# Optimization experiments

Hardware: AMD Instinct MI355X
Metric: run time of the kernel (lower is better)

## Reference

```python
import jax, jax.numpy as jnp
import numpy as np

N_QUBITS = 16
NUM_CLASSES = 16
C64 = jnp.complex64


def rx_mat(theta):
    # RX(theta) = [[cos(t/2), -i sin(t/2)], [-i sin(t/2), cos(t/2)]]
    c = jnp.cos(theta / 2).astype(C64)
    s = jnp.sin(theta / 2).astype(C64)
    row0 = jnp.stack([c, -1j * s], axis=-1)
    row1 = jnp.stack([-1j * s, c], axis=-1)
    return jnp.stack([row0, row1], axis=-2)  # (..., 2, 2)


def rot_mat(phi, theta, omega):
    # PennyLane Rot = RZ(omega) RY(theta) RZ(phi)
    c = jnp.cos(theta / 2).astype(C64)
    s = jnp.sin(theta / 2).astype(C64)
    phi = phi.astype(C64)
    omega = omega.astype(C64)
    e_m = jnp.exp(-0.5j * (phi + omega))
    e_p = jnp.exp(0.5j * (phi + omega))
    e_d = jnp.exp(0.5j * (phi - omega))
    e_dm = jnp.exp(-0.5j * (phi - omega))
    return jnp.array([[e_m * c, -e_d * s], [e_dm * s, e_p * c]], dtype=C64)


def apply_1q(state, U, w):
    # state: (B, 2, ..., 2) with qubit w at axis 1+w; U: (2,2) or (B,2,2)
    s = jnp.moveaxis(state, 1 + w, -1)
    if U.ndim == 3:
        s = jnp.einsum('b...i,bji->b...j', s, U)
    else:
        s = jnp.einsum('...i,ji->...j', s, U)
    return jnp.moveaxis(s, -1, 1 + w)


def apply_crx(state, theta, ctrl, tgt):
    U = rx_mat(theta)  # (2, 2)
    s = jnp.moveaxis(state, (1 + ctrl, 1 + tgt), (-2, -1))
    s1 = jnp.einsum('...i,ji->...j', s[..., 1, :], U)
    s = jnp.stack([s[..., 0, :], s1], axis=-2)
    return jnp.moveaxis(s, (-2, -1), (1 + ctrl, 1 + tgt))


def circuit(feats, rot1, crx1, rot2, crx2):
    # feats: (B, 16) rotation angles (data re-uploading)
    B = feats.shape[0]
    state = jnp.zeros((B,) + (2,) * N_QUBITS, dtype=C64)
    state = state.at[(slice(None),) + (0,) * N_QUBITS].set(1.0)

    def layer(state, rot_w, crx_w):
        for i in range(N_QUBITS):
            state = apply_1q(state, rx_mat(feats[:, i]), i)  # batched RX
        for i in range(N_QUBITS):
            state = apply_1q(state, rot_mat(rot_w[i, 0], rot_w[i, 1], rot_w[i, 2]), i)
        for i in range(N_QUBITS):
            state = apply_crx(state, crx_w[i], i, (i + 1) % N_QUBITS)
        return state

    state = layer(state, rot1, crx1)
    state = layer(state, rot2, crx2)

    probs = (state.real ** 2 + state.imag ** 2)  # (B, 2, ..., 2) float32
    evs = []
    for i in range(N_QUBITS):
        p = jnp.moveaxis(probs, 1 + i, 1).reshape(B, 2, -1).sum(-1)
        evs.append(p[:, 0] - p[:, 1])  # <Z_i>
    return jnp.stack(evs, axis=1)  # (B, 16)


def adaptive_pool_441(x):
    # AdaptiveAvgPool3d((4,4,1)) with divisible dims -> block means
    B, C, D, H, W = x.shape
    x = x.reshape(B, C, 4, D // 4, 4, H // 4, 1, W)
    return x.mean(axis=(3, 5, 7))  # (B, C, 4, 4, 1)


def setup_inputs() -> dict:
    key = jax.random.key(0)
    ks = jax.random.split(key, 9)
    B = 128
    x = jax.random.normal(ks[0], (B, 2, 16, 64, 64), dtype=jnp.float32)
    compress_w = jax.random.normal(ks[1], (N_QUBITS, 32), jnp.float32) * 0.1
    compress_b = jax.random.normal(ks[2], (N_QUBITS,), jnp.float32) * 0.01
    rot1 = jax.random.normal(ks[3], (N_QUBITS, 3), jnp.float32) * 0.1
    crx1 = jax.random.normal(ks[4], (N_QUBITS,), jnp.float32) * 0.1
    rot2 = jax.random.normal(ks[5], (N_QUBITS, 3), jnp.float32) * 0.1
    crx2 = jax.random.normal(ks[6], (N_QUBITS,), jnp.float32) * 0.1
    fc_w = jax.random.normal(ks[7], (NUM_CLASSES, N_QUBITS), jnp.float32) * 0.1
    fc_b = jax.random.normal(ks[8], (NUM_CLASSES,), jnp.float32) * 0.01
    return {"x": x, "compress_w": compress_w, "compress_b": compress_b,
            "rot1": rot1, "crx1": crx1, "rot2": rot2, "crx2": crx2,
            "fc_w": fc_w, "fc_b": fc_b}


def reference(x, compress_w, compress_b, rot1, crx1, rot2, crx2, fc_w, fc_b):
    B = x.shape[0]
    p = adaptive_pool_441(x).reshape(B, -1)          # (B, 32)
    feats = p @ compress_w.T + compress_b            # (B, 16)
    q_out = circuit(feats, rot1, crx1, rot2, crx2)   # (B, 16)
    logits = q_out @ fc_w.T + fc_b                   # (B, 16)
    return jax.nn.log_softmax(logits, axis=1)
```

## Files before the change

kernel.cpp:

```cpp
#include <hip/hip_runtime.h>
#include <hip/hip_bf16.h>

typedef float f2 __attribute__((ext_vector_type(2)));

__device__ __forceinline__ f2 sgate(f2 a, int lane, int kt, int kc, const float* u) {
    f2 p;
    p.x = __shfl_xor(a.x, 1 << kt);
    p.y = __shfl_xor(a.y, 1 << kt);
    const float* uu = u + ((kc >= 0 && ((lane >> kc) & 1)) ? 8 : 0);
    int bit = (lane >> kt) & 1;
    float cAr = bit ? uu[6] : uu[0], cAi = bit ? uu[7] : uu[1];
    float cPr = bit ? uu[4] : uu[2], cPi = bit ? uu[5] : uu[3];
    f2 r;
    r.x = cAr * a.x - cAi * a.y + cPr * p.x - cPi * p.y;
    r.y = cAr * a.y + cAi * a.x + cPr * p.y + cPi * p.x;
    return r;
}

__device__ __forceinline__ f2 cmul(f2 A, f2 B) {
    return f2{A.x * B.x - A.y * B.y, A.x * B.y + A.y * B.x};
}
__device__ __forceinline__ f2 cmulc(f2 x, f2 y) {
    return f2{x.x * y.x + x.y * y.y, x.y * y.x - x.x * y.y};
}

__global__ __launch_bounds__(256) void pool_kernel(const float* __restrict__ x,
                                                   float* __restrict__ p) {
    int blk = blockIdx.x;
    int b = blk >> 5, j = blk & 31;
    int c = j >> 4, dd = (j >> 2) & 3, hh = j & 3;
    const float4* xb = (const float4*)(x + (((size_t)(b * 2 + c) * 16 + dd * 4) << 12)
                                         + (size_t)hh * 1024);
    int tid = threadIdx.x;
    float sum = 0.f;
    #pragma unroll
    for (int k = 0; k < 4; ++k) {
        int f = k * 256 + tid;
        int r = f >> 4, col = f & 15;
        int off = (r >> 4) * 1024 + (r & 15) * 16 + col;
        float4 v = xb[off];
        sum += v.x + v.y + v.z + v.w;
    }
    #pragma unroll
    for (int o = 1; o < 64; o <<= 1) sum += __shfl_xor(sum, o);
    __shared__ float red[4];
    if ((tid & 63) == 0) red[tid >> 6] = sum;
    __syncthreads();
    if (tid == 0) p[blk] = (red[0] + red[1] + red[2] + red[3]) * (1.0f / 4096.0f);
}

__global__ __launch_bounds__(256) void qfin(const float* __restrict__ p,
                                            const float* __restrict__ cw,
                                            const float* __restrict__ cb,
                                            const float* __restrict__ rot1,
                                            const float* __restrict__ crx1,
                                            const float* __restrict__ rot2,
                                            const float* __restrict__ crx2,
                                            const float* __restrict__ fcw,
                                            const float* __restrict__ fcb,
                                            float* __restrict__ out) {
    __shared__ float pp[32];
    __shared__ float uM[32][16];
    __shared__ float cs15[4];
    __shared__ f2 ell[64];
    __shared__ f2 Rr[2][64];
    __shared__ f2 Wl[2][32];
    __shared__ f2 Btab[4][64];
    __shared__ f2 Ctab[8][32];
    __shared__ float Rtab[2][4][64];
    __shared__ float sH[2][6][32];
    __shared__ float sD[2][32];
    __shared__ float sE[2][32];
    __shared__ float redP[4][7];
    __shared__ float redQ[4][8];
    __shared__ float evf[16];
    __shared__ float lgf[16];
    int tid = threadIdx.x;
    int b = blockIdx.x;

    if (tid < 32) pp[tid] = p[b * 32 + tid];
    __syncthreads();

    if (tid < 32) {
        int q = tid & 15, l = tid >> 4;
        float f = cb[q];
        #pragma unroll
        for (int jj = 0; jj < 32; ++jj) f += pp[jj] * cw[q * 32 + jj];
        float cr = cosf(0.5f * f), sr = sinf(0.5f * f);
        const float* rw = (l == 0 ? rot1 : rot2) + q * 3;
        float phi = rw[0], th = rw[1], om = rw[2];
        float ct = cosf(0.5f * th), st = sinf(0.5f * th);
        float aa = 0.5f * (phi + om), dd = 0.5f * (phi - om);
        float ca = cosf(aa), sa = sinf(aa), cd = cosf(dd), sd = sinf(dd);
        float R00r =  ct * ca, R00i = -ct * sa;
        float R01r = -st * cd, R01i = -st * sd;
        float R10r =  st * cd, R10i = -st * sd;
        float R11r =  ct * ca, R11i =  ct * sa;
        float u0 = cr * R00r + sr * R01i;
        float u1 = cr * R00i - sr * R01r;
        float u2 = cr * R01r + sr * R00i;
        float u3 = cr * R01i - sr * R00r;
        float u4 = cr * R10r + sr * R11i;
        float u5 = cr * R10i - sr * R11r;
        float u6 = cr * R11r + sr * R10i;
        float u7 = cr * R11i - sr * R10r;
        float g[16];
        g[0] = u0; g[1] = u1; g[2] = u2; g[3] = u3;
        g[4] = u4; g[5] = u5; g[6] = u6; g[7] = u7;
        if (q >= 1) {
            float thc = (l == 0 ? crx1 : crx2)[q - 1];
            float c2 = cosf(0.5f * thc), s2 = sinf(0.5f * thc);
            g[8]  = c2*u0 + s2*u5;  g[9]  = c2*u1 - s2*u4;
            g[10] = c2*u2 + s2*u7;  g[11] = c2*u3 - s2*u6;
            g[12] = c2*u4 + s2*u1;  g[13] = c2*u5 - s2*u0;
            g[14] = c2*u6 + s2*u3;  g[15] = c2*u7 - s2*u2;
        } else {
            #pragma unroll
            for (int k = 0; k < 8; ++k) g[8 + k] = g[k];
        }
        float* s = uM[l * 16 + q];
        #pragma unroll
        for (int k = 0; k < 16; ++k) s[k] = g[k];
        if (q == 15) {
            float th2 = (l == 0 ? crx1 : crx2)[15];
            cs15[l * 2]     = cosf(0.5f * th2);
            cs15[l * 2 + 1] = sinf(0.5f * th2);
        }
    }
    __syncthreads();

    int wv = tid >> 6, lane = tid & 63;

    if (wv == 0) {
        f2 a = (lane == 0) ? f2{1.f, 0.f} : f2{0.f, 0.f};
        a = sgate(a, lane, 0, -1, uM[0]);
        #pragma unroll
        for (int q = 1; q <= 5; ++q) a = sgate(a, lane, q, q - 1, uM[q]);
        ell[lane] = a;
    } else if (wv <= 2) {
        int pidx = wv - 1;
        const float* m6 = uM[6] + pidx * 8;
        f2 a = f2{0.f, 0.f};
        if (lane == 0) a = f2{m6[0], m6[1]};
        if (lane == 1) a = f2{m6[4], m6[5]};
        #pragma unroll
        for (int q = 7; q <= 11; ++q) a = sgate(a, lane, q - 6, q - 7, uM[q]);
        Rr[pidx][lane] = a;
    } else {
        int j = lane >> 5, lm = lane & 31;
        f2 a = (lm == j) ? f2{1.f, 0.f} : f2{0.f, 0.f};
        #pragma unroll
        for (int q = 12; q <= 15; ++q) a = sgate(a, lane, q - 11, q - 12, uM[q]);
        Wl[j][lm] = a;
    }
    __syncthreads();

    {
        int c = wv >> 1, pb = wv & 1;
        f2 a = ell[lane];
        if (((lane >> 5) & 1) != pb) a = f2{0.f, 0.f};
        if (c) {
            f2 pr; pr.x = __shfl_xor(a.x, 1); pr.y = __shfl_xor(a.y, 1);
            f2 n = cs15[0] * a;
            n.x += cs15[1] * pr.y; n.y -= cs15[1] * pr.x;
            a = n;
        }
        a = sgate(a, lane, 0, -1, uM[16]);
        #pragma unroll
        for (int q = 1; q <= 5; ++q) a = sgate(a, lane, q, q - 1, uM[16 + q]);
        Btab[wv][lane] = a;
    }
    {
        int pidx = wv >> 1, p2 = wv & 1, j = lane >> 5, lm = lane & 31;
        f2 a = Rr[pidx][(j << 5) | lm];
        a = sgate(a, lane, 0, -1, uM[16 + 6] + p2 * 8);
        #pragma unroll
        for (int q = 7; q <= 10; ++q) a = sgate(a, lane, q - 6, q - 7, uM[16 + q]);
        Ctab[(pidx * 2 + j) * 2 + p2][lm] = a;
    }
    {
        int c = wv >> 1, bsel = wv & 1, j = lane >> 5, lm = lane & 31;
        f2 a = Wl[j][lm];
        if (((lm >> 4) & 1) != c) a = f2{0.f, 0.f};
        a = sgate(a, lane, 0, -1, uM[16 + 11] + bsel * 8);
        #pragma unroll
        for (int q = 12; q <= 15; ++q) a = sgate(a, lane, q - 11, q - 12, uM[16 + q]);
        Rtab[bsel][c * 2 + j][2 * lm]     = a.x;
        Rtab[bsel][c * 2 + j][2 * lm + 1] = a.y;
    }
    __syncthreads();

    if (tid < 192) {
        int bsel = tid / 96, rem = tid % 96, pt = rem >> 4, kk = rem & 15;
        int k = kk >> 2, k2 = kk & 3;
        float c15 = cs15[2], s15 = cs15[3];
        f2 Elo = f2{0.f, 0.f}, Ehi = f2{0.f, 0.f};
        #pragma unroll
        for (int m = 0; m < 32; ++m) {
            float rk = Rtab[bsel][k][2 * m],  ik = Rtab[bsel][k][2 * m + 1];
            float rp = Rtab[bsel][k2][2 * m], ip = Rtab[bsel][k2][2 * m + 1];
            float sg = (pt == 0) ? 1.f : (((m >> (pt - 1)) & 1) ? -1.f : 1.f);
            float wr = sg * (rk * rp + ik * ip);
            float wi = sg * (ik * rp - rk * ip);
            if (m < 16) { Elo.x += wr; Elo.y += wi; }
            else        { Ehi.x += wr; Ehi.y += wi; }
        }
        sH[bsel][pt][2 * kk]     = Elo.x + Ehi.x;
        sH[bsel][pt][2 * kk + 1] = Elo.y + Ehi.y;
        if (pt == 0) {
            float ccss = c15 * c15 - s15 * s15;
            sD[bsel][2 * kk]     = Elo.x + ccss * Ehi.x;
            sD[bsel][2 * kk + 1] = Elo.y + ccss * Ehi.y;
            float cs = c15 * s15;
            sE[bsel][2 * kk]     = cs * Ehi.x;
            sE[bsel][2 * kk + 1] = cs * Ehi.y;
        }
    }
    __syncthreads();

    int x0 = 2 * (tid & 31), x1 = x0 + 1;
    int x5 = (tid >> 4) & 1;

    f2 B0[2][2], B1[2][2];
    #pragma unroll
    for (int c = 0; c < 2; ++c)
        #pragma unroll
        for (int pq = 0; pq < 2; ++pq) {
            B0[c][pq] = Btab[c * 2 + pq][x0];
            B1[c][pq] = Btab[c * 2 + pq][x1];
        }

    float Pa = 0.f, P9 = 0.f, P10 = 0.f, Pd = 0.f;
    float S0 = 0.f, S1 = 0.f, S2 = 0.f, S3 = 0.f, S4 = 0.f;

    for (int part = 0; part < 4; ++part) {
        int bsel = part >> 1;
        int y = part * 8 + (tid >> 5);
        f2 Cv[2][2];
        #pragma unroll
        for (int pq = 0; pq < 2; ++pq)
            #pragma unroll
            for (int j = 0; j < 2; ++j)
                Cv[pq][j] = Ctab[(pq * 2 + j) * 2 + x5][y];

        f2 a[4], bb[4];
        #pragma unroll
        for (int c = 0; c < 2; ++c)
            #pragma unroll
            for (int j = 0; j < 2; ++j) {
                f2 s0 = cmul(B0[c][0], Cv[0][j]);
                f2 s1 = cmul(B0[c][1], Cv[1][j]);
                a[c * 2 + j] = f2{s0.x + s1.x, s0.y + s1.y};
                f2 t0 = cmul(B1[c][0], Cv[0][j]);
                f2 t1 = cmul(B1[c][1], Cv[1][j]);
                bb[c * 2 + j] = f2{t0.x + t1.x, t0.y + t1.y};
            }

        float sum_d[4], dif_d[4];
        #pragma unroll
        for (int k = 0; k < 4; ++k) {
            float pa = a[k].x * a[k].x + a[k].y * a[k].y;
            float pb = bb[k].x * bb[k].x + bb[k].y * bb[k].y;
            sum_d[k] = pa + pb;
            dif_d[k] = pa - pb;
        }
        f2 wS[6], wD[6];
        {
            int pi = 0;
            #pragma unroll
            for (int k = 0; k < 4; ++k)
                #pragma unroll
                for (int k2 = k + 1; k2 < 4; ++k2) {
                    f2 u = cmulc(a[k], a[k2]);
                    f2 v = cmulc(bb[k], bb[k2]);
                    wS[pi] = f2{u.x + v.x, u.y + v.y};
                    wD[pi] = f2{u.x - v.x, u.y - v.y};
                    ++pi;
                }
        }

        float F[6];
        #pragma unroll
        for (int pt = 0; pt < 6; ++pt) {
            const float* Hk = sH[bsel][pt];
            float f = 0.f;
            #pragma unroll
            for (int k = 0; k < 4; ++k) f += Hk[(k * 4 + k) * 2] * sum_d[k];
            int pi = 0;
            #pragma unroll
            for (int k = 0; k < 4; ++k)
                #pragma unroll
                for (int k2 = k + 1; k2 < 4; ++k2) {
                    float hr = Hk[(k * 4 + k2) * 2], hi = Hk[(k * 4 + k2) * 2 + 1];
                    f += 2.f * (hr * wS[pi].x - hi * wS[pi].y);
                    ++pi;
                }
            F[pt] = f;
        }
        float pd_i;
        {
            const float* Dk = sD[bsel];
            const float* Ek = sE[bsel];
            float f = 0.f;
            #pragma unroll
            for (int k = 0; k < 4; ++k) f += Dk[(k * 4 + k) * 2] * dif_d[k];
            int pi = 0;
            #pragma unroll
            for (int k = 0; k < 4; ++k)
                #pragma unroll
                for (int k2 = k + 1; k2 < 4; ++k2) {
                    float dr = Dk[(k * 4 + k2) * 2], di = Dk[(k * 4 + k2) * 2 + 1];
                    f += 2.f * (dr * wD[pi].x - di * wD[pi].y);
                    ++pi;
                }
            f2 z = f2{0.f, 0.f};
            #pragma unroll
            for (int k = 0; k < 4; ++k) {
                f2 v = f2{0.f, 0.f};
                #pragma unroll
                for (int k2 = 0; k2 < 4; ++k2) {
                    float er = Ek[(k * 4 + k2) * 2], ei = Ek[(k * 4 + k2) * 2 + 1];
                    v.x += er * bb[k2].x + ei * bb[k2].y;
                    v.y += ei * bb[k2].x - er * bb[k2].y;
                }
                z.x += a[k].x * v.x - a[k].y * v.y;
                z.y += a[k].x * v.y + a[k].y * v.x;
            }
            pd_i = f - 4.f * z.y;
        }

        Pa  += F[0];
        P9  += (part & 1) ? -F[0] : F[0];
        P10 += (part & 2) ? -F[0] : F[0];
        Pd  += pd_i;
        S0 += F[1]; S1 += F[2]; S2 += F[3]; S3 += F[4]; S4 += F[5];
    }

    #pragma unroll
    for (int o = 1; o < 64; o <<= 1) {
        float tP = __shfl_xor(Pa, o);
        Pa = (lane & o) ? (tP - Pa) : (Pa + tP);
        Pd  += __shfl_xor(Pd, o);
        P9  += __shfl_xor(P9, o);
        P10 += __shfl_xor(P10, o);
        S0  += __shfl_xor(S0, o);
        S1  += __shfl_xor(S1, o);
        S2  += __shfl_xor(S2, o);
        S3  += __shfl_xor(S3, o);
        S4  += __shfl_xor(S4, o);
    }
    if ((lane & (lane - 1)) == 0) {
        int slot = (lane == 0) ? 0 : (31 - __clz((unsigned)lane)) + 1;
        redP[wv][slot] = Pa;
    }
    if (lane == 0) {
        redQ[wv][0] = Pd;  redQ[wv][1] = P9;  redQ[wv][2] = P10;
        redQ[wv][3] = S0;  redQ[wv][4] = S1;  redQ[wv][5] = S2;
        redQ[wv][6] = S3;  redQ[wv][7] = S4;
    }
    __syncthreads();
    if (tid < 16) {
        int q = tid;
        float v;
        if (q == 0)      v = redQ[0][0] + redQ[1][0] + redQ[2][0] + redQ[3][0];
        else if (q < 7)  v = redP[0][q] + redP[1][q] + redP[2][q] + redP[3][q];
        else if (q == 7) v = redP[0][0] - redP[1][0] + redP[2][0] - redP[3][0];
        else if (q == 8) v = redP[0][0] + redP[1][0] - redP[2][0] - redP[3][0];
        else if (q == 9)  v = redQ[0][1] + redQ[1][1] + redQ[2][1] + redQ[3][1];
        else if (q == 10) v = redQ[0][2] + redQ[1][2] + redQ[2][2] + redQ[3][2];
        else              v = redQ[0][q-8] + redQ[1][q-8] + redQ[2][q-8] + redQ[3][q-8];
        evf[q] = v;
    }
    __syncthreads();

    if (tid < 16) {
        int c = tid;
        float v = fcb[c];
        #pragma unroll
        for (int q = 0; q < 16; ++q) v += evf[q] * fcw[c * 16 + q];
        lgf[c] = v;
    }
    __syncthreads();
    if (tid < 16) {
        float mx = -1e30f;
        #pragma unroll
        for (int c2 = 0; c2 < 16; ++c2) mx = fmaxf(mx, lgf[c2]);
        float se = 0.f;
        #pragma unroll
        for (int c2 = 0; c2 < 16; ++c2) se += expf(lgf[c2] - mx);
        out[b * 16 + tid] = lgf[tid] - (mx + logf(se));
    }
}

extern "C" void kernel_launch(void* const* d_in, const int* in_sizes, int n_in,
                              void* d_out, int out_size, void* d_ws, size_t ws_size,
                              hipStream_t stream) {
    const float* x    = (const float*)d_in[0];
    const float* cw   = (const float*)d_in[1];
    const float* cb   = (const float*)d_in[2];
    const float* rot1 = (const float*)d_in[3];
    const float* crx1 = (const float*)d_in[4];
    const float* rot2 = (const float*)d_in[5];
    const float* crx2 = (const float*)d_in[6];
    const float* fcw  = (const float*)d_in[7];
    const float* fcb  = (const float*)d_in[8];

    float* p = (float*)d_ws;

    pool_kernel<<<4096, 256, 0, stream>>>(x, p);
    qfin<<<128, 256, 0, stream>>>(p, cw, cb, rot1, crx1, rot2, crx2,
                                  fcw, fcb, (float*)d_out);
}
```

Baseline: 30.91 us.

## Fuse adaptive pooling into quantum circuit kernel, dropping separate pool launch

Removes the standalone pooling kernel and has each block of the circuit kernel pool its own sample's 512KB input directly into shared memory before running the circuit. This eliminates one kernel launch and the workspace round-trip. The cost is that only 128 blocks now stream all 64MB of input, instead of 4096 blocks, so memory-level parallelism and bandwidth use may drop sharply.

New measurement: 27.84 us. -9.9%, faster.

```diff
diff --git a/kernel.cpp b/kernel.cpp
--- a/kernel.cpp
+++ b/kernel.cpp
@@ -24,41 +24,16 @@
     return f2{x.x * y.x + x.y * y.y, x.y * y.x - x.x * y.y};
 }
 
-__global__ __launch_bounds__(256) void pool_kernel(const float* __restrict__ x,
-                                                   float* __restrict__ p) {
-    int blk = blockIdx.x;
-    int b = blk >> 5, j = blk & 31;
-    int c = j >> 4, dd = (j >> 2) & 3, hh = j & 3;
-    const float4* xb = (const float4*)(x + (((size_t)(b * 2 + c) * 16 + dd * 4) << 12)
-                                         + (size_t)hh * 1024);
-    int tid = threadIdx.x;
-    float sum = 0.f;
-    #pragma unroll
-    for (int k = 0; k < 4; ++k) {
-        int f = k * 256 + tid;
-        int r = f >> 4, col = f & 15;
-        int off = (r >> 4) * 1024 + (r & 15) * 16 + col;
-        float4 v = xb[off];
-        sum += v.x + v.y + v.z + v.w;
-    }
-    #pragma unroll
-    for (int o = 1; o < 64; o <<= 1) sum += __shfl_xor(sum, o);
-    __shared__ float red[4];
-    if ((tid & 63) == 0) red[tid >> 6] = sum;
-    __syncthreads();
-    if (tid == 0) p[blk] = (red[0] + red[1] + red[2] + red[3]) * (1.0f / 4096.0f);
-}
-
-__global__ __launch_bounds__(256) void qfin(const float* __restrict__ p,
-                                            const float* __restrict__ cw,
-                                            const float* __restrict__ cb,
-                                            const float* __restrict__ rot1,
-                                            const float* __restrict__ crx1,
-                                            const float* __restrict__ rot2,
-                                            const float* __restrict__ crx2,
-                                            const float* __restrict__ fcw,
-                                            const float* __restrict__ fcb,
-                                            float* __restrict__ out) {
+__global__ __launch_bounds__(256) void qall2(const float* __restrict__ x,
+                                             const float* __restrict__ cw,
+                                             const float* __restrict__ cb,
+                                             const float* __restrict__ rot1,
+                                             const float* __restrict__ crx1,
+                                             const float* __restrict__ rot2,
+                                             const float* __restrict__ crx2,
+                                             const float* __restrict__ fcw,
+                                             const float* __restrict__ fcb,
+                                             float* __restrict__ out) {
     __shared__ float pp[32];
     __shared__ float uM[32][16];
     __shared__ float cs15[4];
@@ -78,7 +53,26 @@
     int tid = threadIdx.x;
     int b = blockIdx.x;
 
-    if (tid < 32) pp[tid] = p[b * 32 + tid];
+    {
+        int g = tid >> 3, sub = tid & 7;
+        int c = g >> 4, dd = (g >> 2) & 3, hh = g & 3;
+        const float4* xb = (const float4*)(x + (size_t)b * 131072)
+                         + c * 16384 + dd * 4096 + hh * 256;
+        float sum = 0.f;
+        #pragma unroll
+        for (int d = 0; d < 4; ++d) {
+            const float4* ch = xb + d * 1024;
+            #pragma unroll 8
+            for (int i = 0; i < 32; ++i) {
+                float4 v = ch[i * 8 + sub];
+                sum += v.x + v.y + v.z + v.w;
+            }
+        }
+        sum += __shfl_xor(sum, 1);
+        sum += __shfl_xor(sum, 2);
+        sum += __shfl_xor(sum, 4);
+        if (sub == 0) pp[g] = sum * (1.0f / 4096.0f);
+    }
     __syncthreads();
 
     if (tid < 32) {
@@ -405,9 +399,6 @@
     const float* fcw  = (const float*)d_in[7];
     const float* fcb  = (const float*)d_in[8];
 
-    float* p = (float*)d_ws;
-
-    pool_kernel<<<4096, 256, 0, stream>>>(x, p);
-    qfin<<<128, 256, 0, stream>>>(p, cw, cb, rot1, crx1, rot2, crx2,
-                                  fcw, fcb, (float*)d_out);
+    qall2<<<128, 256, 0, stream>>>(x, cw, cb, rot1, crx1, rot2, crx2,
+                                   fcw, fcb, (float*)d_out);
 }
```
